# Kernel tuning notes

Hardware: AMD Instinct MI355X
Metric: run time of the kernel (lower is better)

Reference implementation:

```python
import jax, jax.numpy as jnp
import numpy as np


def _mha(x, pos, wq, bq, wk, bk, wv, bv, num_heads):
    # x: (B, S, Din); pos: (S, Din); w*: (Din, Dout); b*: (Dout,)
    x = x + pos  # learned positional embedding, broadcast over batch
    q = x @ wq + bq
    k = x @ wk + bk
    v = x @ wv + bv
    B, S, O = q.shape
    hd = O // num_heads
    q = q.reshape(B, S, num_heads, hd)
    k = k.reshape(B, S, num_heads, hd)
    v = v.reshape(B, S, num_heads, hd)
    scores = jnp.einsum('bshd,bthd->bhst', q, k) / jnp.sqrt(jnp.asarray(hd, x.dtype))
    attn = jax.nn.softmax(scores, axis=-1)
    out = jnp.einsum('bhst,bthd->bshd', attn, v)
    return out.reshape(B, S, O)


def setup_inputs() -> dict:
    key = jax.random.key(0)
    ks = jax.random.split(key, 16)
    B = 16384
    s = 0.3
    f32 = jnp.float32
    return {
        'state': jax.random.normal(ks[0], (B, 100), f32),
        # intraframe attention: Din=1, Dout=2, seq=10, heads=2
        'pos_intra': jax.random.normal(ks[1], (10, 1), f32) * s,
        'wq_intra': jax.random.normal(ks[2], (1, 2), f32) * s,
        'bq_intra': jnp.zeros((2,), f32),
        'wk_intra': jax.random.normal(ks[3], (1, 2), f32) * s,
        'bk_intra': jnp.zeros((2,), f32),
        'wv_intra': jax.random.normal(ks[4], (1, 2), f32) * s,
        'bv_intra': jnp.zeros((2,), f32),
        # interframe attention: Din=20, Dout=21, seq=10, heads=1
        'pos_inter': jax.random.normal(ks[5], (10, 20), f32) * s,
        'wq_inter': jax.random.normal(ks[6], (20, 21), f32) * s,
        'bq_inter': jnp.zeros((21,), f32),
        'wk_inter': jax.random.normal(ks[7], (20, 21), f32) * s,
        'bk_inter': jnp.zeros((21,), f32),
        'wv_inter': jax.random.normal(ks[8], (20, 21), f32) * s,
        'bv_inter': jnp.zeros((21,), f32),
    }


def reference(state, pos_intra, wq_intra, bq_intra, wk_intra, bk_intra,
              wv_intra, bv_intra, pos_inter, wq_inter, bq_inter, wk_inter,
              bk_inter, wv_inter, bv_inter):
    B = state.shape[0]
    # per-sample reshape (10,10,1) fused across the batch: (B*10 frames, 10 tokens, 1 feat)
    frames = state.reshape(B * 10, 10, 1)
    intra = _mha(frames, pos_intra, wq_intra, bq_intra, wk_intra, bk_intra,
                 wv_intra, bv_intra, num_heads=2)          # (B*10, 10, 2)
    x = intra.reshape(B, 10, 20)                            # (B, frames=10, 20)
    out = _mha(x, pos_inter, wq_inter, bq_inter, wk_inter, bk_inter,
               wv_inter, bv_inter, num_heads=1)             # (B, 10, 21)
    return out
```

## Files before the change

kernel.cpp:

```cpp
#include <hip/hip_runtime.h>

typedef __fp16 h2 __attribute__((ext_vector_type(2)));
typedef __fp16 h4 __attribute__((ext_vector_type(4)));
typedef __fp16 h8 __attribute__((ext_vector_type(8)));
typedef float  f4 __attribute__((ext_vector_type(4)));
typedef float  f2 __attribute__((ext_vector_type(2)));

#if __has_builtin(__builtin_amdgcn_fdot2)
#define FDOT2(a, b, c) __builtin_amdgcn_fdot2((a), (b), (c), false)
#else
#define FDOT2(a, b, c) ((c) + (float)(a)[0] * (float)(b)[0] + (float)(a)[1] * (float)(b)[1])
#endif

#define SPB 16
#define NT  320

__device__ __forceinline__ float dpp_xor1(float x) {
    int i = __builtin_amdgcn_mov_dpp(__float_as_int(x), 0xB1, 0xF, 0xF, true);
    return __int_as_float(i);
}

struct SMa {
    __fp16 X [160 * 32];
    __fp16 WT[96 * 32];
};
union UHead { SMa a; float sout[SPB * 210]; };

__global__ __launch_bounds__(NT, 5)
void crazy_attn_kernel(const float* __restrict__ state,
                       const float* __restrict__ pos_intra,
                       const float* __restrict__ wq_i, const float* __restrict__ bq_i,
                       const float* __restrict__ wk_i, const float* __restrict__ bk_i,
                       const float* __restrict__ wv_i, const float* __restrict__ bv_i,
                       const float* __restrict__ pos_inter,
                       const float* __restrict__ wq, const float* __restrict__ bq,
                       const float* __restrict__ wk, const float* __restrict__ bk,
                       const float* __restrict__ wv, const float* __restrict__ bv,
                       float* __restrict__ out, int B)
{
    __shared__ UHead uh;
    __shared__ __fp16 QKV[160 * 72];

    const int tid  = threadIdx.x;
    const int e    = tid & 1;
    const int rr   = (tid >> 1) % 10;
    const int samp = tid / 20;
    const int gs   = blockIdx.x * SPB + samp;
    const int gsc  = (gs < B) ? gs : (B - 1);

    float xv[10];
    {
        const float* sp = state + (size_t)gsc * 100 + rr * 10;
        #pragma unroll
        for (int t2 = 0; t2 < 5; ++t2) {
            const f2 v = *(const f2*)&sp[t2 * 2];
            xv[2 * t2]     = v[0] + pos_intra[2 * t2];
            xv[2 * t2 + 1] = v[1] + pos_intra[2 * t2 + 1];
        }
    }
    float xmx = xv[0], xmn = xv[0];
    #pragma unroll
    for (int t = 1; t < 10; ++t) { xmx = fmaxf(xmx, xv[t]); xmn = fminf(xmn, xv[t]); }

    if (tid < 96) {
        const int sec = tid >> 5, within = tid & 31;
        const bool valid = within < 21;
        const float* W  = (sec == 1) ? wk : (sec == 2) ? wv : wq;
        const float* Bb = (sec == 1) ? bk : (sec == 2) ? bv : bq;
        union { uint4 u4[4]; h2 hh[16]; } T;
        #pragma unroll
        for (int p = 0; p < 16; ++p) {
            const int j0 = 2 * p, j1 = 2 * p + 1;
            float lo = 0.f, hi = 0.f;
            if (valid) {
                lo = (j0 < 20) ? W[j0 * 21 + within] : ((j0 == 20) ? Bb[within] : 0.f);
                hi = (j1 < 20) ? W[j1 * 21 + within] : 0.f;
            }
            T.hh[p] = __builtin_amdgcn_cvt_pkrtz(lo, hi);
        }
        uint4* wd = (uint4*)&uh.a.WT[tid * 32];
        wd[0] = T.u4[0]; wd[1] = T.u4[1]; wd[2] = T.u4[2]; wd[3] = T.u4[3];
    }
    __syncthreads();

    {
        float res[2][5];
        #pragma unroll
        for (int h = 0; h < 2; ++h) {
            const float wqh = wq_i[h], bqh = bq_i[h];
            const float wkh = wk_i[h];
            const float wvh = wv_i[h], bvh = bv_i[h];
            float vh[10];
            #pragma unroll
            for (int t = 0; t < 10; ++t) vh[t] = fmaf(xv[t], wvh, bvh);
            #pragma unroll
            for (int si = 0; si < 5; ++si) {
                const float c0 = fmaf(xv[2 * si],     wqh, bqh) * wkh;
                const float c1 = fmaf(xv[2 * si + 1], wqh, bqh) * wkh;
                const float c  = e ? c1 : c0;
                const float mx = c * ((c >= 0.f) ? xmx : xmn);
                const float cL = c * 1.44269504f;
                const float mL = mx * 1.44269504f;
                float s0a = 0.f, s0b = 0.f, o0a = 0.f, o0b = 0.f;
                #pragma unroll
                for (int t = 0; t < 5; ++t) {
                    const float ea_ = __builtin_amdgcn_exp2f(fmaf(cL, xv[2 * t],     -mL));
                    const float eb_ = __builtin_amdgcn_exp2f(fmaf(cL, xv[2 * t + 1], -mL));
                    s0a += ea_;                  s0b += eb_;
                    o0a = fmaf(ea_, vh[2 * t], o0a);
                    o0b = fmaf(eb_, vh[2 * t + 1], o0b);
                }
                res[h][si] = (o0a + o0b) * __builtin_amdgcn_rcpf(s0a + s0b);
            }
        }
        __fp16* xrow = &uh.a.X[(samp * 10 + rr) * 32];
        const float* prow = pos_inter + rr * 20;
        #pragma unroll
        for (int si = 0; si < 5; ++si) {
            const int s = 2 * si + e;
            *(h2*)&xrow[2 * s] = __builtin_amdgcn_cvt_pkrtz(res[0][si] + prow[2 * s],
                                                            res[1][si] + prow[2 * s + 1]);
        }
        const h2 z  = __builtin_amdgcn_cvt_pkrtz(0.f, 0.f);
        const h2 bz = __builtin_amdgcn_cvt_pkrtz(1.0f, 0.f);
        #pragma unroll
        for (int j = 0; j < 3; ++j) {
            const int k = 20 + 2 * (3 * e + j);
            *(h2*)&xrow[k] = (e == 0 && j == 0) ? bz : z;
        }
    }

    {
        const int l  = tid & 63;
        const int w  = tid >> 6;
        const int lr = l & 15, lh = l >> 4;
        h8 afrag[6];
        #pragma unroll
        for (int mt = 0; mt < 6; ++mt)
            afrag[mt] = *(const h8*)&uh.a.WT[(mt * 16 + lr) * 32 + lh * 8];
        #pragma unroll
        for (int i = 0; i < 2; ++i) {
            const int xrow = (2 * w + i) * 16 + lr;
            const h8 bfrag = *(const h8*)&uh.a.X[xrow * 32 + lh * 8];
            #pragma unroll
            for (int mt = 0; mt < 6; ++mt) {
                f4 acc = {0.f, 0.f, 0.f, 0.f};
                acc = __builtin_amdgcn_mfma_f32_16x16x32_f16(afrag[mt], bfrag, acc, 0, 0, 0);
                const int m0     = mt * 16 + lh * 4;
                const int sec    = m0 >> 5;
                const int within = m0 & 31;
                if (within <= 20) {
                    union { h2 p2[2]; h4 p4; } P;
                    P.p2[0] = __builtin_amdgcn_cvt_pkrtz(acc[0], acc[1]);
                    P.p2[1] = __builtin_amdgcn_cvt_pkrtz(acc[2], acc[3]);
                    *(h4*)&QKV[xrow * 72 + sec * 24 + within] = P.p4;
                }
            }
        }
    }
    __syncthreads();

    {
        const __fp16* samprows = &QKV[samp * 10 * 72];
        union { uint4 u4[3]; h2 hh[12]; } Q;
        {
            const uint4* qsrc = (const uint4*)&samprows[rr * 72];
            Q.u4[0] = qsrc[0]; Q.u4[1] = qsrc[1]; Q.u4[2] = qsrc[2];
        }
        float mysc[5];
        #pragma unroll
        for (int i = 0; i < 5; ++i) {
            const int t = 2 * i + e;
            union { uint4 u4[3]; h2 hh[12]; } K;
            const uint4* ks = (const uint4*)&samprows[t * 72 + 24];
            K.u4[0] = ks[0]; K.u4[1] = ks[1]; K.u4[2] = ks[2];
            float d = 0.f;
            #pragma unroll
            for (int p = 0; p < 11; ++p) d = FDOT2(Q.hh[p], K.hh[p], d);
            mysc[i] = d * 0.21821789023599239f;
        }
        float mymax = mysc[0];
        #pragma unroll
        for (int i = 1; i < 5; ++i) mymax = fmaxf(mymax, mysc[i]);
        const float m = fmaxf(mymax, dpp_xor1(mymax));
        float pe[5], psum = 0.f;
        #pragma unroll
        for (int i = 0; i < 5; ++i) {
            pe[i] = __builtin_amdgcn_exp2f((mysc[i] - m) * 1.44269504f);
            psum += pe[i];
        }
        const float sum = psum + dpp_xor1(psum);
        const float inv = __builtin_amdgcn_rcpf(sum);

        float acc[21];
        #pragma unroll
        for (int c = 0; c < 21; ++c) acc[c] = 0.f;
        #pragma unroll
        for (int i = 0; i < 5; ++i) {
            const int t = 2 * i + e;
            union { uint4 u4[3]; h2 hh[12]; } V;
            const uint4* vs = (const uint4*)&samprows[t * 72 + 48];
            V.u4[0] = vs[0]; V.u4[1] = vs[1]; V.u4[2] = vs[2];
            const float a = pe[i] * inv;
            #pragma unroll
            for (int c = 0; c < 21; ++c)
                acc[c] = fmaf(a, (float)V.hh[c >> 1][c & 1], acc[c]);
        }
        #pragma unroll
        for (int c = 0; c < 21; ++c) acc[c] += dpp_xor1(acc[c]);
        if (e == 0) {
            float* dst = &uh.sout[(samp * 10 + rr) * 21];
            #pragma unroll
            for (int c = 0; c < 21; ++c) dst[c] = acc[c];
        }
    }
    __syncthreads();

    {
        const int samp0 = blockIdx.x * SPB;
        const int nrem  = B - samp0;
        const int nval  = ((nrem < SPB) ? nrem : SPB) * 210;
        float* gdst = out + (size_t)samp0 * 210;
        if (nval == SPB * 210) {
            for (int i = tid; i < SPB * 210 / 4; i += NT)
                ((f4*)gdst)[i] = ((const f4*)uh.sout)[i];
        } else {
            for (int i = tid; i < nval; i += NT) gdst[i] = uh.sout[i];
        }
    }
}

extern "C" void kernel_launch(void* const* d_in, const int* in_sizes, int n_in,
                              void* d_out, int out_size, void* d_ws, size_t ws_size,
                              hipStream_t stream) {
    const float* state     = (const float*)d_in[0];
    const float* pos_intra = (const float*)d_in[1];
    const float* wq_i      = (const float*)d_in[2];
    const float* bq_i      = (const float*)d_in[3];
    const float* wk_i      = (const float*)d_in[4];
    const float* bk_i      = (const float*)d_in[5];
    const float* wv_i      = (const float*)d_in[6];
    const float* bv_i      = (const float*)d_in[7];
    const float* pos_inter = (const float*)d_in[8];
    const float* wq        = (const float*)d_in[9];
    const float* bq        = (const float*)d_in[10];
    const float* wk        = (const float*)d_in[11];
    const float* bk        = (const float*)d_in[12];
    const float* wv        = (const float*)d_in[13];
    const float* bv        = (const float*)d_in[14];
    float* outp = (float*)d_out;

    const int B = in_sizes[0] / 100;
    const int grid = (B + SPB - 1) / SPB;
    hipLaunchKernelGGL(crazy_attn_kernel, dim3(grid), dim3(NT), 0, stream,
                       state, pos_intra, wq_i, bq_i, wk_i, bk_i, wv_i, bv_i,
                       pos_inter, wq, bq, wk, bk, wv, bv, outp, B);
}
```

Before: 22.48 us.

## Process two sample groups per block with software-pipelined stages

Each block now handles two groups of 16 samples, with separate shared-memory buffers for each group. The stages are interleaved: group 1 is loaded and its intra-attention runs between the projections of group 0, and group 0's output is written while group 1's inter-attention computes. Per block this loads and converts the weight matrix once for 32 samples instead of 16, and it halves the grid. It also folds the intra value projection algebraically into one final fma. The costs are larger shared memory, launch bounds lowered to 2 blocks, and fewer blocks to hide latency.

```diff
diff --git a/kernel.cpp b/kernel.cpp
--- a/kernel.cpp
+++ b/kernel.cpp
@@ -12,7 +12,8 @@
 #define FDOT2(a, b, c) ((c) + (float)(a)[0] * (float)(b)[0] + (float)(a)[1] * (float)(b)[1])
 #endif
 
-#define SPB 16
+#define SPG 16
+#define SPB 32
 #define NT  320
 
 __device__ __forceinline__ float dpp_xor1(float x) {
@@ -20,13 +21,9 @@
     return __int_as_float(i);
 }
 
-struct SMa {
-    __fp16 X [160 * 32];
-    __fp16 WT[96 * 32];
-};
-union UHead { SMa a; float sout[SPB * 210]; };
-
-__global__ __launch_bounds__(NT, 5)
+#define SM_HALFS 36352
+
+__global__ __launch_bounds__(NT, 2)
 void crazy_attn_kernel(const float* __restrict__ state,
                        const float* __restrict__ pos_intra,
                        const float* __restrict__ wq_i, const float* __restrict__ bq_i,
@@ -38,18 +35,24 @@
                        const float* __restrict__ wv, const float* __restrict__ bv,
                        float* __restrict__ out, int B)
 {
-    __shared__ UHead uh;
-    __shared__ __fp16 QKV[160 * 72];
+    __shared__ __attribute__((aligned(16))) __fp16 SM[SM_HALFS];
+    __fp16* X0   = SM;
+    __fp16* WT   = SM + 5120;
+    __fp16* X1   = SM + 8192;
+    __fp16* QKV0 = SM + 13312;
+    __fp16* QKV1 = SM + 24832;
+    float*  sout0 = (float*)SM;
+    float*  sout1 = (float*)(SM + 8192);
 
     const int tid  = threadIdx.x;
     const int e    = tid & 1;
     const int rr   = (tid >> 1) % 10;
     const int samp = tid / 20;
-    const int gs   = blockIdx.x * SPB + samp;
-    const int gsc  = (gs < B) ? gs : (B - 1);
-
-    float xv[10];
-    {
+    const int gs0  = blockIdx.x * SPB + samp;
+    const int gs1  = gs0 + SPG;
+
+    auto loadXV = [&](int gs, float* xv) {
+        const int gsc = (gs < B) ? gs : (B - 1);
         const float* sp = state + (size_t)gsc * 100 + rr * 10;
         #pragma unroll
         for (int t2 = 0; t2 < 5; ++t2) {
@@ -57,42 +60,18 @@
             xv[2 * t2]     = v[0] + pos_intra[2 * t2];
             xv[2 * t2 + 1] = v[1] + pos_intra[2 * t2 + 1];
         }
-    }
-    float xmx = xv[0], xmn = xv[0];
-    #pragma unroll
-    for (int t = 1; t < 10; ++t) { xmx = fmaxf(xmx, xv[t]); xmn = fminf(xmn, xv[t]); }
-
-    if (tid < 96) {
-        const int sec = tid >> 5, within = tid & 31;
-        const bool valid = within < 21;
-        const float* W  = (sec == 1) ? wk : (sec == 2) ? wv : wq;
-        const float* Bb = (sec == 1) ? bk : (sec == 2) ? bv : bq;
-        union { uint4 u4[4]; h2 hh[16]; } T;
-        #pragma unroll
-        for (int p = 0; p < 16; ++p) {
-            const int j0 = 2 * p, j1 = 2 * p + 1;
-            float lo = 0.f, hi = 0.f;
-            if (valid) {
-                lo = (j0 < 20) ? W[j0 * 21 + within] : ((j0 == 20) ? Bb[within] : 0.f);
-                hi = (j1 < 20) ? W[j1 * 21 + within] : 0.f;
-            }
-            T.hh[p] = __builtin_amdgcn_cvt_pkrtz(lo, hi);
-        }
-        uint4* wd = (uint4*)&uh.a.WT[tid * 32];
-        wd[0] = T.u4[0]; wd[1] = T.u4[1]; wd[2] = T.u4[2]; wd[3] = T.u4[3];
-    }
-    __syncthreads();
-
-    {
+    };
+
+    auto stageA = [&](const float* xv, __fp16* Xb) {
+        float xmx = xv[0], xmn = xv[0];
+        #pragma unroll
+        for (int t = 1; t < 10; ++t) { xmx = fmaxf(xmx, xv[t]); xmn = fminf(xmn, xv[t]); }
         float res[2][5];
         #pragma unroll
         for (int h = 0; h < 2; ++h) {
             const float wqh = wq_i[h], bqh = bq_i[h];
             const float wkh = wk_i[h];
             const float wvh = wv_i[h], bvh = bv_i[h];
-            float vh[10];
-            #pragma unroll
-            for (int t = 0; t < 10; ++t) vh[t] = fmaf(xv[t], wvh, bvh);
             #pragma unroll
             for (int si = 0; si < 5; ++si) {
                 const float c0 = fmaf(xv[2 * si],     wqh, bqh) * wkh;
@@ -106,14 +85,14 @@
                 for (int t = 0; t < 5; ++t) {
                     const float ea_ = __builtin_amdgcn_exp2f(fmaf(cL, xv[2 * t],     -mL));
                     const float eb_ = __builtin_amdgcn_exp2f(fmaf(cL, xv[2 * t + 1], -mL));
-                    s0a += ea_;                  s0b += eb_;
-                    o0a = fmaf(ea_, vh[2 * t], o0a);
-                    o0b = fmaf(eb_, vh[2 * t + 1], o0b);
+                    s0a += ea_;                      s0b += eb_;
+                    o0a = fmaf(ea_, xv[2 * t],     o0a);
+                    o0b = fmaf(eb_, xv[2 * t + 1], o0b);
                 }
-                res[h][si] = (o0a + o0b) * __builtin_amdgcn_rcpf(s0a + s0b);
+                res[h][si] = fmaf(wvh, (o0a + o0b) * __builtin_amdgcn_rcpf(s0a + s0b), bvh);
             }
         }
-        __fp16* xrow = &uh.a.X[(samp * 10 + rr) * 32];
+        __fp16* xrow = &Xb[(samp * 10 + rr) * 32];
         const float* prow = pos_inter + rr * 20;
         #pragma unroll
         for (int si = 0; si < 5; ++si) {
@@ -128,20 +107,20 @@
             const int k = 20 + 2 * (3 * e + j);
             *(h2*)&xrow[k] = (e == 0 && j == 0) ? bz : z;
         }
-    }
-
-    {
+    };
+
+    auto stageB = [&](const __fp16* Xb, __fp16* QKVb) {
         const int l  = tid & 63;
         const int w  = tid >> 6;
         const int lr = l & 15, lh = l >> 4;
         h8 afrag[6];
         #pragma unroll
         for (int mt = 0; mt < 6; ++mt)
-            afrag[mt] = *(const h8*)&uh.a.WT[(mt * 16 + lr) * 32 + lh * 8];
+            afrag[mt] = *(const h8*)&WT[(mt * 16 + lr) * 32 + lh * 8];
         #pragma unroll
         for (int i = 0; i < 2; ++i) {
             const int xrow = (2 * w + i) * 16 + lr;
-            const h8 bfrag = *(const h8*)&uh.a.X[xrow * 32 + lh * 8];
+            const h8 bfrag = *(const h8*)&Xb[xrow * 32 + lh * 8];
             #pragma unroll
             for (int mt = 0; mt < 6; ++mt) {
                 f4 acc = {0.f, 0.f, 0.f, 0.f};
@@ -153,15 +132,14 @@
                     union { h2 p2[2]; h4 p4; } P;
                     P.p2[0] = __builtin_amdgcn_cvt_pkrtz(acc[0], acc[1]);
                     P.p2[1] = __builtin_amdgcn_cvt_pkrtz(acc[2], acc[3]);
-                    *(h4*)&QKV[xrow * 72 + sec * 24 + within] = P.p4;
+                    *(h4*)&QKVb[xrow * 72 + sec * 24 + within] = P.p4;
                 }
             }
         }
-    }
-    __syncthreads();
-
-    {
-        const __fp16* samprows = &QKV[samp * 10 * 72];
+    };
+
+    auto stageC = [&](const __fp16* QKVb, float* soutb) {
+        const __fp16* samprows = &QKVb[samp * 720];
         union { uint4 u4[3]; h2 hh[12]; } Q;
         {
             const uint4* qsrc = (const uint4*)&samprows[rr * 72];
@@ -209,25 +187,66 @@
         #pragma unroll
         for (int c = 0; c < 21; ++c) acc[c] += dpp_xor1(acc[c]);
         if (e == 0) {
-            float* dst = &uh.sout[(samp * 10 + rr) * 21];
+            float* dst = &soutb[(samp * 10 + rr) * 21];
             #pragma unroll
             for (int c = 0; c < 21; ++c) dst[c] = acc[c];
         }
+    };
+
+    auto epi = [&](const float* soutb, int sample0) {
+        const int nrem = B - sample0;
+        const int nval = ((nrem < SPG) ? (nrem < 0 ? 0 : nrem) : SPG) * 210;
+        float* gdst = out + (size_t)sample0 * 210;
+        if (nval == SPG * 210) {
+            for (int i = tid; i < SPG * 210 / 4; i += NT)
+                ((f4*)gdst)[i] = ((const f4*)soutb)[i];
+        } else {
+            for (int i = tid; i < nval; i += NT) gdst[i] = soutb[i];
+        }
+    };
+
+    float xv0[10];
+    loadXV(gs0, xv0);
+
+    if (tid < 96) {
+        const int sec = tid >> 5, within = tid & 31;
+        const bool valid = within < 21;
+        const float* W  = (sec == 1) ? wk : (sec == 2) ? wv : wq;
+        const float* Bb = (sec == 1) ? bk : (sec == 2) ? bv : bq;
+        union { uint4 u4[4]; h2 hh[16]; } T;
+        #pragma unroll
+        for (int p = 0; p < 16; ++p) {
+            const int j0 = 2 * p, j1 = 2 * p + 1;
+            float lo = 0.f, hi = 0.f;
+            if (valid) {
+                lo = (j0 < 20) ? W[j0 * 21 + within] : ((j0 == 20) ? Bb[within] : 0.f);
+                hi = (j1 < 20) ? W[j1 * 21 + within] : 0.f;
+            }
+            T.hh[p] = __builtin_amdgcn_cvt_pkrtz(lo, hi);
+        }
+        uint4* wd = (uint4*)&WT[tid * 32];
+        wd[0] = T.u4[0]; wd[1] = T.u4[1]; wd[2] = T.u4[2]; wd[3] = T.u4[3];
     }
-    __syncthreads();
-
-    {
-        const int samp0 = blockIdx.x * SPB;
-        const int nrem  = B - samp0;
-        const int nval  = ((nrem < SPB) ? nrem : SPB) * 210;
-        float* gdst = out + (size_t)samp0 * 210;
-        if (nval == SPB * 210) {
-            for (int i = tid; i < SPB * 210 / 4; i += NT)
-                ((f4*)gdst)[i] = ((const f4*)uh.sout)[i];
-        } else {
-            for (int i = tid; i < nval; i += NT) gdst[i] = uh.sout[i];
-        }
-    }
+
+    stageA(xv0, X0);
+    __syncthreads();
+
+    float xv1[10];
+    loadXV(gs1, xv1);
+
+    stageB(X0, QKV0);
+    stageA(xv1, X1);
+    stageB(X1, QKV1);
+    __syncthreads();
+
+    stageC(QKV0, sout0);
+    __syncthreads();
+
+    epi(sout0, blockIdx.x * SPB);
+    stageC(QKV1, sout1);
+    __syncthreads();
+
+    epi(sout1, blockIdx.x * SPB + SPG);
 }
 
 extern "C" void kernel_launch(void* const* d_in, const int* in_sizes, int n_in,
```

After: 26.35 us. +17.2%, slower.
